# Optimization experiments

Hardware: AMD Instinct MI355X
Metric: run time of the kernel (lower is better)

The kernel has to match this reference:

```python
import jax, jax.numpy as jnp
import numpy as np

B, T, S = 128, 500, 200   # batch, seq_len, num_skills
E, H = 100, 100           # embed_dim, lstm hidden


def setup_inputs() -> dict:
    key = jax.random.key(0)
    ks = jax.random.split(key, 8)
    skill = jax.random.randint(ks[0], (B, T), 0, S)
    bit = jax.random.randint(ks[1], (B, T), 0, 2)
    # one-hot interaction: position 2*skill + (0 if correct else 1)
    x = jax.nn.one_hot(skill * 2 + bit, 2 * S, dtype=jnp.float32)
    qi = jax.random.randint(ks[2], (B, T), 0, S)
    q = jax.nn.one_hot(qi, S, dtype=jnp.float32)
    delta = jnp.zeros((B, T, 1), jnp.float32)  # unused in no_tempo model
    Wx = jax.random.normal(ks[3], (2 * S, E), jnp.float32) * 0.05
    bx = jnp.zeros((E,), jnp.float32)
    # LSTM input dim = E + 3 (correct/incorrect/total count feats)
    lstm_k = jax.random.normal(ks[4], (E + 3, 4 * H), jnp.float32) * 0.05
    lstm_rk = jax.random.normal(ks[5], (H, 4 * H), jnp.float32) * 0.05
    # keras unit_forget_bias: forget-gate bias section = 1 (gate order i,f,c,o)
    lstm_b = jnp.concatenate([jnp.zeros(H), jnp.ones(H), jnp.zeros(2 * H)]).astype(jnp.float32)
    Wo = jax.random.normal(ks[6], (H, S), jnp.float32) * 0.05
    bo = jnp.zeros((S,), jnp.float32)
    return {"x": x, "delta": delta, "q": q, "Wx": Wx, "bx": bx,
            "lstm_k": lstm_k, "lstm_rk": lstm_rk, "lstm_b": lstm_b,
            "Wo": Wo, "bo": bo}


def _forward(x, q, Wx, bx, lstm_k, lstm_rk, lstm_b, Wo, bo):
    mask = jnp.any(x != 0, axis=-1)              # [B,T] keras Masking(0)
    embed_x = x @ Wx + bx                        # [B,T,E]
    xt = jnp.swapaxes(x, 0, 1)                   # [T,B,2S]
    mt = jnp.swapaxes(mask, 0, 1)                # [T,B]

    # CountStateRNNCell: state = sum(x_t)*prev + x_t ; masked steps pass state through
    def count_step(c, inp):
        x_t, m_t = inp
        new = jnp.sum(x_t, axis=-1, keepdims=True) * c + x_t
        c = jnp.where(m_t[:, None], new, c)
        return c, c

    c0 = jnp.zeros((x.shape[0], x.shape[-1]), x.dtype)
    _, counts = jax.lax.scan(count_step, c0, (xt, mt))
    count_t = jnp.log1p(jnp.swapaxes(counts, 0, 1))  # [B,T,2S]

    idx = jnp.argmax(x, axis=-1) // 2                # skill index [B,T]
    # one_hot * count + reduce_sum  ==  gather
    cc = jnp.take_along_axis(count_t, (idx * 2)[..., None], axis=-1)      # correct
    ic = jnp.take_along_axis(count_t, (idx * 2 + 1)[..., None], axis=-1)  # incorrect
    # count_format='binary' hits the typo'd else-branch -> all_count (3 feats)
    count_feat = jnp.concatenate([cc, ic, cc + ic], axis=-1)              # [B,T,3]

    x_c_t = jnp.concatenate([embed_x, count_feat], axis=-1)               # [B,T,E+3]
    zt = jnp.swapaxes(x_c_t @ lstm_k + lstm_b, 0, 1)                      # [T,B,4H]

    def lstm_step(carry, inp):
        h, c = carry
        z_t, m_t = inp
        z = z_t + h @ lstm_rk
        i, f, g, o = jnp.split(z, 4, axis=-1)
        c_new = jax.nn.sigmoid(f) * c + jax.nn.sigmoid(i) * jnp.tanh(g)
        h_new = jax.nn.sigmoid(o) * jnp.tanh(c_new)
        m = m_t[:, None]
        h = jnp.where(m, h_new, h)
        c = jnp.where(m, c_new, c)
        return (h, c), h

    h0 = jnp.zeros((x.shape[0], H), x.dtype)
    _, hs = jax.lax.scan(lstm_step, (h0, h0), (zt, mt))
    h_seq = jnp.swapaxes(hs, 0, 1)                                        # [B,T,H]

    # dropout = identity (inference); Dense(1, kernel=1, bias=0) = sum over skills
    y = jax.nn.sigmoid(h_seq @ Wo + bo) * q
    return jnp.sum(y, axis=-1, keepdims=True)                             # [B,T,1]


def reference(x, delta, q, Wx, bx, lstm_k, lstm_rk, lstm_b, Wo, bo):
    return _forward(x, q, Wx, bx, lstm_k, lstm_rk, lstm_b, Wo, bo)
```

## Files before the change

### kernel.cpp

```cpp
#include <hip/hip_runtime.h>
#include <hip/hip_bf16.h>
#include <hip/hip_fp16.h>

#define TB 128
#define TT 500
#define TS 200
#define TE 100
#define TH 100
#define NCLS 400
#define NG   400
#define BT   (TB*TT)
#define BLK  448

typedef _Float16 h8 __attribute__((ext_vector_type(8)));
union HU { float4 f4; __half hs[8]; };

__device__ __forceinline__ float frcp(float x) { return __builtin_amdgcn_rcpf(x); }
__device__ __forceinline__ float fsig(float x) { return frcp(1.f + __expf(-x)); }
__device__ __forceinline__ float ftanh(float x) { float e = __expf(2.f * x); return 1.f - 2.f * frcp(e + 1.f); }

__device__ __forceinline__ void barrier_lds() {
  asm volatile("s_waitcnt lgkmcnt(0)\n\ts_barrier" ::: "memory");
}

#define QXOR1(d, s) d = __int_as_float(__builtin_amdgcn_mov_dpp(__float_as_int(s), 177, 0xf, 0xf, true))
#define QXOR2(d, s) d = __int_as_float(__builtin_amdgcn_mov_dpp(__float_as_int(s),  78, 0xf, 0xf, true))
#define QXOR3(d, s) d = __int_as_float(__builtin_amdgcn_mov_dpp(__float_as_int(s),  27, 0xf, 0xf, true))

__global__ void k_compress(const float* __restrict__ x, const float* __restrict__ q,
                           int* __restrict__ idx2, int* __restrict__ qi) {
  int gid  = blockIdx.x * blockDim.x + threadIdx.x;
  int wave = gid >> 6;
  int lane = threadIdx.x & 63;
  if (wave >= BT) return;

  const float4* xr = (const float4*)(x + (size_t)wave * NCLS);
  int li = -1;
  {
    float4 v = xr[lane];
    if (v.x > 0.5f) li = lane * 4 + 0;
    if (v.y > 0.5f) li = lane * 4 + 1;
    if (v.z > 0.5f) li = lane * 4 + 2;
    if (v.w > 0.5f) li = lane * 4 + 3;
    int ci = 64 + lane;
    if (ci < 100) {
      float4 w = xr[ci];
      if (w.x > 0.5f) li = ci * 4 + 0;
      if (w.y > 0.5f) li = ci * 4 + 1;
      if (w.z > 0.5f) li = ci * 4 + 2;
      if (w.w > 0.5f) li = ci * 4 + 3;
    }
  }
  #pragma unroll
  for (int off = 32; off; off >>= 1) li = max(li, __shfl_xor(li, off));

  const float4* qr = (const float4*)(q + (size_t)wave * TS);
  int qj = -1;
  if (lane < 50) {
    float4 v = qr[lane];
    if (v.x > 0.5f) qj = lane * 4 + 0;
    if (v.y > 0.5f) qj = lane * 4 + 1;
    if (v.z > 0.5f) qj = lane * 4 + 2;
    if (v.w > 0.5f) qj = lane * 4 + 3;
  }
  #pragma unroll
  for (int off = 32; off; off >>= 1) qj = max(qj, __shfl_xor(qj, off));

  if (lane == 0) { idx2[wave] = li; qi[wave] = qj; }
}

__global__ void k_counts(const int* __restrict__ idx2, float2* __restrict__ ccg) {
  __shared__ int ids[TT];
  int b = blockIdx.x, tid = threadIdx.x;
  for (int i = tid; i < TT; i += 512) ids[i] = idx2[(size_t)b * TT + i];
  __syncthreads();
  if (tid < TT) {
    int s2 = ids[tid] & ~1;
    int c0 = 0, c1 = 0;
    for (int tp = 0; tp <= tid; ++tp) {
      int v = ids[tp];
      c0 += (v == s2);
      c1 += (v == s2 + 1);
    }
    ccg[(size_t)b * TT + tid] =
        make_float2(__logf(1.f + (float)c0), __logf(1.f + (float)c1));
  }
}

__global__ void k_precompute(const float* __restrict__ Wx, const float* __restrict__ bx,
                             const float* __restrict__ K, const float* __restrict__ lb,
                             const float* __restrict__ Wo, const float* __restrict__ R,
                             float* __restrict__ Gq, float* __restrict__ baseq,
                             float* __restrict__ c0q, float* __restrict__ c1q,
                             float* __restrict__ WoT, float4* __restrict__ Bfrag) {
  int bid = blockIdx.x, tid = threadIdx.x;
  if (bid < NCLS) {
    if (tid < NG) {
      float acc = 0.0f;
      for (int e = 0; e < TE; ++e) acc = fmaf(Wx[bid * TE + e], K[e * NG + tid], acc);
      int g = tid / 100, u = tid % 100;
      int cp = (u >> 2) * 16 + (u & 3) * 4 + g;
      Gq[bid * NG + cp] = acc;
    }
  } else if (bid == NCLS) {
    if (tid < NG) {
      float acc = lb[tid];
      for (int e = 0; e < TE; ++e) acc = fmaf(bx[e], K[e * NG + tid], acc);
      int g = tid / 100, u = tid % 100;
      int cp = (u >> 2) * 16 + (u & 3) * 4 + g;
      baseq[cp] = acc;
      c0q[cp]   = K[100 * NG + tid] + K[102 * NG + tid];
      c1q[cp]   = K[101 * NG + tid] + K[102 * NG + tid];
    }
  } else {
    int id = (bid - NCLS - 1) * 512 + tid;
    if (id < TS * TH) {
      int s = id / TH, k = id % TH;
      WoT[id] = Wo[k * TS + s];
    } else {
      int id2 = id - TS * TH;
      if (id2 < 6400) {
        int lane = id2 & 63, ks = (id2 >> 6) & 3, tile = id2 >> 8;
        int qq = lane & 15, cgrp = lane >> 4;
        int col = (qq & 3) * 100 + tile * 4 + (qq >> 2);
        HU uu;
        #pragma unroll
        for (int j = 0; j < 8; ++j) {
          int k = ks * 32 + cgrp * 8 + j;
          float v = (k < TH) ? R[k * NG + col] : 0.0f;
          uu.hs[j] = __float2half_rn(v);
        }
        Bfrag[id2] = uu.f4;
      }
    }
  }
}

#define AW(N, V) asm volatile("v_accvgpr_write_b32 a" #N ", %0" :: "v"(V) : "a" #N)
#define AW4(N0,N1,N2,N3, F) do { AW(N0,(F).x); AW(N1,(F).y); AW(N2,(F).z); AW(N3,(F).w); } while(0)

#define CLOBS \
  "a0","a1","a2","a3","a4","a5","a6","a7","a8","a9","a10","a11","a12","a13", \
  "a14","a15","a16","a17","a18","a19","a20","a21","a22","a23","a24","a25",   \
  "a26","a27","a28","a29","a30","a31","a32","a33","a34","a35","a36","a37",   \
  "a38","a39","a40","a41","a42","a43","a44","a45","a46","a47","a48","a49",   \
  "a50","a51","a52","a53","a54","a55","a56","a57","a58","a59","a60","a61",   \
  "a62","a63","a64","a65","a66","a67","a68","a69","a70","a71","a72","a73",   \
  "a74","a75","a76","a77","a78","a79","a80","a81","a82","a83"

#define MFMA16(Z0,Z1,Z2,Z3, FA0,FA1,FA2,FA3)                          \
  asm volatile(                                                       \
    "s_nop 1\n\t"                                                     \
    "v_mfma_f32_16x16x32_f16 a[64:67], %4, a[0:3],   a[80:83]\n\t"    \
    "v_mfma_f32_16x16x32_f16 a[68:71], %4, a[16:19], a[80:83]\n\t"    \
    "v_mfma_f32_16x16x32_f16 a[72:75], %4, a[32:35], a[80:83]\n\t"    \
    "v_mfma_f32_16x16x32_f16 a[76:79], %4, a[48:51], a[80:83]\n\t"    \
    "v_mfma_f32_16x16x32_f16 a[64:67], %5, a[4:7],   a[64:67]\n\t"    \
    "v_mfma_f32_16x16x32_f16 a[68:71], %5, a[20:23], a[68:71]\n\t"    \
    "v_mfma_f32_16x16x32_f16 a[72:75], %5, a[36:39], a[72:75]\n\t"    \
    "v_mfma_f32_16x16x32_f16 a[76:79], %5, a[52:55], a[76:79]\n\t"    \
    "v_mfma_f32_16x16x32_f16 a[64:67], %6, a[8:11],  a[64:67]\n\t"    \
    "v_mfma_f32_16x16x32_f16 a[68:71], %6, a[24:27], a[68:71]\n\t"    \
    "v_mfma_f32_16x16x32_f16 a[72:75], %6, a[40:43], a[72:75]\n\t"    \
    "v_mfma_f32_16x16x32_f16 a[76:79], %6, a[56:59], a[76:79]\n\t"    \
    "v_mfma_f32_16x16x32_f16 a[64:67], %7, a[12:15], a[64:67]\n\t"    \
    "v_mfma_f32_16x16x32_f16 a[68:71], %7, a[28:31], a[68:71]\n\t"    \
    "v_mfma_f32_16x16x32_f16 a[72:75], %7, a[44:47], a[72:75]\n\t"    \
    "v_mfma_f32_16x16x32_f16 a[76:79], %7, a[60:63], a[76:79]\n\t"    \
    "s_nop 7\n\ts_nop 7\n\ts_nop 7\n\t"                               \
    "v_accvgpr_read_b32 %0, a64\n\t"                                  \
    "v_accvgpr_read_b32 %1, a68\n\t"                                  \
    "v_accvgpr_read_b32 %2, a72\n\t"                                  \
    "v_accvgpr_read_b32 %3, a76"                                      \
    : "=v"(Z0), "=v"(Z1), "=v"(Z2), "=v"(Z3)                          \
    : "v"(FA0), "v"(FA1), "v"(FA2), "v"(FA3)                          \
    : CLOBS)

__global__ void __attribute__((amdgpu_flat_work_group_size(BLK, BLK)))
k_lstm(const int* __restrict__ idx2, const float* __restrict__ Gq,
       const float* __restrict__ baseq, const float* __restrict__ c0q,
       const float* __restrict__ c1q, const float4* __restrict__ Bfrag,
       const float2* __restrict__ ccg, float* __restrict__ h_seq) {
  __shared__ __align__(16) __half hbuf[2][128];
  __shared__ int idx_ls[TT];

  int b = blockIdx.x, tid = threadIdx.x;
  int w = tid >> 6, lane = tid & 63;
  int g3 = lane & 3, cg = lane >> 4, qd = (lane >> 2) & 3;

  for (int i = tid; i < TT; i += BLK) idx_ls[i] = idx2[(size_t)b * TT + i];
  if (tid < 128) { hbuf[0][tid] = __float2half(0.f); hbuf[1][tid] = __float2half(0.f); }

  int tS0 = (w < 6) ? 4 * w     : 24;
  int tS1 = (w < 6) ? 4 * w + 1 : 24;
  int tS2 = (w < 6) ? 4 * w + 2 : 24;
  int tS3 = (w < 6) ? 4 * w + 3 : 24;

  int gcol = (w < 6) ? (64 * w + lane)
                     : (24 * 16 + (lane & 15));
  float basej = baseq[gcol], c0j = c0q[gcol], c1j = c1q[gcol];
  int u_wr = 16 * w + 4 * cg + qd;
  bool wr = (g3 == 0) && (((w < 6) ? u_wr : (96 + qd)) < TH) && !(w == 6 && cg != 0);
  int u_fin = (w < 6) ? u_wr : (96 + qd);

  {
    float4 f;
    f = Bfrag[(tS0 * 4 + 0) * 64 + lane]; AW4(0,1,2,3, f);
    f = Bfrag[(tS0 * 4 + 1) * 64 + lane]; AW4(4,5,6,7, f);
    f = Bfrag[(tS0 * 4 + 2) * 64 + lane]; AW4(8,9,10,11, f);
    f = Bfrag[(tS0 * 4 + 3) * 64 + lane]; AW4(12,13,14,15, f);
    f = Bfrag[(tS1 * 4 + 0) * 64 + lane]; AW4(16,17,18,19, f);
    f = Bfrag[(tS1 * 4 + 1) * 64 + lane]; AW4(20,21,22,23, f);
    f = Bfrag[(tS1 * 4 + 2) * 64 + lane]; AW4(24,25,26,27, f);
    f = Bfrag[(tS1 * 4 + 3) * 64 + lane]; AW4(28,29,30,31, f);
    f = Bfrag[(tS2 * 4 + 0) * 64 + lane]; AW4(32,33,34,35, f);
    f = Bfrag[(tS2 * 4 + 1) * 64 + lane]; AW4(36,37,38,39, f);
    f = Bfrag[(tS2 * 4 + 2) * 64 + lane]; AW4(40,41,42,43, f);
    f = Bfrag[(tS2 * 4 + 3) * 64 + lane]; AW4(44,45,46,47, f);
    f = Bfrag[(tS3 * 4 + 0) * 64 + lane]; AW4(48,49,50,51, f);
    f = Bfrag[(tS3 * 4 + 1) * 64 + lane]; AW4(52,53,54,55, f);
    f = Bfrag[(tS3 * 4 + 2) * 64 + lane]; AW4(56,57,58,59, f);
    f = Bfrag[(tS3 * 4 + 3) * 64 + lane]; AW4(60,61,62,63, f);
    float zf = 0.0f;
    AW(80, zf); AW(81, zf); AW(82, zf); AW(83, zf);
  }
  asm volatile("" ::: CLOBS);

  float c_reg = 0.f;
  __syncthreads();

  const float2* ccg_b = ccg + (size_t)b * TT;
  float gA = Gq[(size_t)idx_ls[0] * NG + gcol];
  float gB = Gq[(size_t)idx_ls[1] * NG + gcol];
  float2 ccA = ccg_b[0], ccB = ccg_b[1];

  float* hout = h_seq + (size_t)b * TT * TH;

  #define STEP(T_, PAR, GV, CCV)                                               \
  { const int t_ = (T_);                                                       \
    barrier_lds();                   \
    const h8* hrow = (const h8*)(&hbuf[(PAR) ^ 1][0]);                         \
    h8 fa0 = hrow[cg], fa1 = hrow[4 + cg], fa2 = hrow[8 + cg], fa3 = hrow[12 + cg]; \
    float z0, z1, z2, z3;                                                      \
    MFMA16(z0, z1, z2, z3, fa0, fa1, fa2, fa3);                                \
    float zlo = (cg & 1) ? z1 : z0;                                            \
    float zhi = (cg & 1) ? z3 : z2;                                            \
    float zsel = (cg & 2) ? zhi : zlo;                                         \
    float2 cc = (CCV);                                                         \
    int tnx = (t_ + 2 < TT) ? t_ + 2 : TT - 1;                                 \
    float z = zsel + (GV) + basej + cc.x * c0j + cc.y * c1j;                   \
    (GV) = Gq[(size_t)idx_ls[tnx] * NG + gcol];          \
    (CCV) = ccg_b[tnx];                                                        \
    float arg = (g3 == 2) ? (z + z) : (-z);                                    \
    float E = __expf(arg);                                                     \
    float r = frcp(1.f + E);                                                   \
    float act = (g3 == 2) ? fmaf(-2.f, r, 1.f) : r;                            \
    float x1, x2, x3;                                                          \
    QXOR1(x1, act); QXOR2(x2, act); QXOR3(x3, act);                            \
    c_reg = fmaf(x1, c_reg, act * x2);               \
    float hn = x3 * ftanh(c_reg);                                              \
    if (wr) {                                                                  \
      hbuf[PAR][u_fin] = __float2half_rn(hn);       \
      hout[(size_t)t_ * TH + u_fin] = hn;                \
    }                                                                          \
  }

  for (int t2 = 0; t2 < TT; t2 += 2) {
    STEP(t2, 0, gA, ccA);
    STEP(t2 + 1, 1, gB, ccB);
  }
  #undef STEP
}

__global__ void k_out(const float* __restrict__ h_seq, const float* __restrict__ WoT,
                      const float* __restrict__ bo, const int* __restrict__ qi,
                      float* __restrict__ out) {
  int gid  = blockIdx.x * blockDim.x + threadIdx.x;
  int wave = gid >> 6;
  int lane = threadIdx.x & 63;
  if (wave >= BT) return;
  int s = qi[wave];
  const float4* h4 = (const float4*)(h_seq + (size_t)wave * TH);
  const float4* w4 = (const float4*)(WoT + (size_t)s * TH);
  float acc = 0.0f;
  if (lane < TH / 4) {
    float4 h = h4[lane];
    float4 w = w4[lane];
    acc = h.x * w.x + h.y * w.y + h.z * w.z + h.w * w.w;
  }
  #pragma unroll
  for (int off = 32; off; off >>= 1) acc += __shfl_xor(acc, off);
  if (lane == 0) out[wave] = fsig(acc + bo[s]);
}

extern "C" void kernel_launch(void* const* d_in, const int* in_sizes, int n_in,
                              void* d_out, int out_size, void* d_ws, size_t ws_size,
                              hipStream_t stream) {
  const float* x    = (const float*)d_in[0];
  const float* q    = (const float*)d_in[2];
  const float* Wx   = (const float*)d_in[3];
  const float* bx   = (const float*)d_in[4];
  const float* K    = (const float*)d_in[5];
  const float* R    = (const float*)d_in[6];
  const float* lb   = (const float*)d_in[7];
  const float* Wo   = (const float*)d_in[8];
  const float* bo   = (const float*)d_in[9];
  float* out = (float*)d_out;

  float* ws = (float*)d_ws;
  float*  Gq     = ws;
  float*  baseq  = ws + 160000;
  float*  c0q    = ws + 160400;
  float*  c1q    = ws + 160800;
  float*  WoT    = ws + 161200;
  float4* Bfrag  = (float4*)(ws + 181200);
  int*    idx2   = (int*)(ws + 206800);
  int*    qi     = (int*)(ws + 270800);
  float2* ccg    = (float2*)(ws + 334800);
  float*  h_seq  = ws + 462800;

  k_compress<<<BT / 4, 256, 0, stream>>>(x, q, idx2, qi);

  k_counts<<<TB, 512, 0, stream>>>(idx2, ccg);

  int tail_blocks = (TS * TH + 6400 + 511) / 512;
  k_precompute<<<NCLS + 1 + tail_blocks, 512, 0, stream>>>(Wx, bx, K, lb, Wo, R,
                                                           Gq, baseq, c0q, c1q, WoT, Bfrag);

  k_lstm<<<TB, BLK, 0, stream>>>(idx2, Gq, baseq, c0q, c1q, Bfrag, ccg, h_seq);

  k_out<<<BT / 4, 256, 0, stream>>>(h_seq, WoT, bo, qi, out);
}
```

Measured before the change: 304.1 us.

## Process two batch sequences per LSTM block using spare MFMA rows

The recurrent LSTM kernel now handles two batch elements per workgroup and launches half as many blocks. The A operand rows of the 16x16 MFMA carry both sequences' hidden states, and each lane runs the gate activations for two outputs. The point is to use MFMA rows that previously computed nothing and to halve the number of serial-recurrence blocks. In exchange each lane does twice the elementwise and gather work per step, and only 64 blocks are active on the GPU.

New measurement: 361.2 us. 18.8% more time.

```diff
diff --git a/kernel.cpp b/kernel.cpp
--- a/kernel.cpp
+++ b/kernel.cpp
@@ -181,27 +181,33 @@
        const float* __restrict__ baseq, const float* __restrict__ c0q,
        const float* __restrict__ c1q, const float4* __restrict__ Bfrag,
        const float2* __restrict__ ccg, float* __restrict__ h_seq) {
-  __shared__ __align__(16) __half hbuf[2][128];
-  __shared__ int idx_ls[TT];
-
-  int b = blockIdx.x, tid = threadIdx.x;
+  __shared__ __align__(16) __half hbuf[2][2][128];
+  __shared__ int idx_ls[2][TT];
+
+  int bid = blockIdx.x, tid = threadIdx.x;
   int w = tid >> 6, lane = tid & 63;
-  int g3 = lane & 3, cg = lane >> 4, qd = (lane >> 2) & 3;
-
-  for (int i = tid; i < TT; i += BLK) idx_ls[i] = idx2[(size_t)b * TT + i];
-  if (tid < 128) { hbuf[0][tid] = __float2half(0.f); hbuf[1][tid] = __float2half(0.f); }
-
-  int tS0 = (w < 6) ? 4 * w     : 24;
-  int tS1 = (w < 6) ? 4 * w + 1 : 24;
-  int tS2 = (w < 6) ? 4 * w + 2 : 24;
-  int tS3 = (w < 6) ? 4 * w + 3 : 24;
-
-  int gcol = (w < 6) ? (64 * w + lane)
-                     : (24 * 16 + (lane & 15));
-  float basej = baseq[gcol], c0j = c0q[gcol], c1j = c1q[gcol];
-  int u_wr = 16 * w + 4 * cg + qd;
-  bool wr = (g3 == 0) && (((w < 6) ? u_wr : (96 + qd)) < TH) && !(w == 6 && cg != 0);
-  int u_fin = (w < 6) ? u_wr : (96 + qd);
+  int q = lane & 15, g3 = lane & 3, cg = lane >> 4, qd = (lane >> 2) & 3;
+  int eA   = (lane >> 3) & 1;
+  int eact = cg >> 1;
+  int s1 = cg & 1, s2 = s1 + 2;
+
+  for (int i = tid; i < TT; i += BLK) {
+    idx_ls[0][i] = idx2[(size_t)(2 * bid) * TT + i];
+    idx_ls[1][i] = idx2[(size_t)(2 * bid + 1) * TT + i];
+  }
+  { __half* hb = &hbuf[0][0][0];
+    for (int i = tid; i < 512; i += BLK) hb[i] = __float2half(0.f); }
+
+  int tS0 = min(4 * w + 0, 24), tS1 = min(4 * w + 1, 24);
+  int tS2 = min(4 * w + 2, 24), tS3 = min(4 * w + 3, 24);
+  int tU1 = 4 * w + s1, tU2 = 4 * w + s2;
+  int tC1 = min(tU1, 24), tC2 = min(tU2, 24);
+  int gcol1 = tC1 * 16 + q, gcol2 = tC2 * 16 + q;
+  float base1 = baseq[gcol1], c01 = c0q[gcol1], c11 = c1q[gcol1];
+  float base2 = baseq[gcol2], c02 = c0q[gcol2], c12 = c1q[gcol2];
+  int u1 = tU1 * 4 + qd, u2 = tU2 * 4 + qd;
+  bool wr1 = (g3 == 0) && (u1 < TH);
+  bool wr2 = (g3 == 0) && (u2 < TH);
 
   {
     float4 f;
@@ -226,50 +232,65 @@
   }
   asm volatile("" ::: CLOBS);
 
-  float c_reg = 0.f;
+  float c_reg1 = 0.f, c_reg2 = 0.f;
   __syncthreads();
 
-  const float2* ccg_b = ccg + (size_t)b * TT;
-  float gA = Gq[(size_t)idx_ls[0] * NG + gcol];
-  float gB = Gq[(size_t)idx_ls[1] * NG + gcol];
-  float2 ccA = ccg_b[0], ccB = ccg_b[1];
-
-  float* hout = h_seq + (size_t)b * TT * TH;
-
-  #define STEP(T_, PAR, GV, CCV)                                               \
-  { const int t_ = (T_);                                                       \
-    barrier_lds();                   \
-    const h8* hrow = (const h8*)(&hbuf[(PAR) ^ 1][0]);                         \
-    h8 fa0 = hrow[cg], fa1 = hrow[4 + cg], fa2 = hrow[8 + cg], fa3 = hrow[12 + cg]; \
-    float z0, z1, z2, z3;                                                      \
-    MFMA16(z0, z1, z2, z3, fa0, fa1, fa2, fa3);                                \
-    float zlo = (cg & 1) ? z1 : z0;                                            \
-    float zhi = (cg & 1) ? z3 : z2;                                            \
-    float zsel = (cg & 2) ? zhi : zlo;                                         \
-    float2 cc = (CCV);                                                         \
-    int tnx = (t_ + 2 < TT) ? t_ + 2 : TT - 1;                                 \
-    float z = zsel + (GV) + basej + cc.x * c0j + cc.y * c1j;                   \
-    (GV) = Gq[(size_t)idx_ls[tnx] * NG + gcol];          \
-    (CCV) = ccg_b[tnx];                                                        \
-    float arg = (g3 == 2) ? (z + z) : (-z);                                    \
+  const int* idxe = idx_ls[eact];
+  const float2* ccg_e = ccg + (size_t)(2 * bid + eact) * TT;
+  float* hout_e = h_seq + (size_t)(2 * bid + eact) * TT * TH;
+
+  float g1A = Gq[(size_t)idxe[0] * NG + gcol1];
+  float g2A = Gq[(size_t)idxe[0] * NG + gcol2];
+  float g1B = Gq[(size_t)idxe[1] * NG + gcol1];
+  float g2B = Gq[(size_t)idxe[1] * NG + gcol2];
+  float2 ccA = ccg_e[0], ccB = ccg_e[1];
+
+  #define ACT(ZZ, CREG, HN)                                                    \
+  { float arg = (g3 == 2) ? ((ZZ) + (ZZ)) : (-(ZZ));                           \
     float E = __expf(arg);                                                     \
     float r = frcp(1.f + E);                                                   \
     float act = (g3 == 2) ? fmaf(-2.f, r, 1.f) : r;                            \
     float x1, x2, x3;                                                          \
     QXOR1(x1, act); QXOR2(x2, act); QXOR3(x3, act);                            \
-    c_reg = fmaf(x1, c_reg, act * x2);               \
-    float hn = x3 * ftanh(c_reg);                                              \
-    if (wr) {                                                                  \
-      hbuf[PAR][u_fin] = __float2half_rn(hn);       \
-      hout[(size_t)t_ * TH + u_fin] = hn;                \
+    (CREG) = fmaf(x1, (CREG), act * x2);   \
+    (HN) = x3 * ftanh(CREG); }
+
+  #define STEP(T_, PAR, G1, G2, CCV)                                           \
+  { const int t_ = (T_);                                                       \
+    barrier_lds();                   \
+    const h8* hrowA = (const h8*)(&hbuf[eA][(PAR) ^ 1][0]);                    \
+    h8 fa0 = hrowA[cg], fa1 = hrowA[4 + cg], fa2 = hrowA[8 + cg], fa3 = hrowA[12 + cg]; \
+    float z0, z1, z2, z3;                                                      \
+    MFMA16(z0, z1, z2, z3, fa0, fa1, fa2, fa3);                                \
+    float zs1 = s1 ? z1 : z0;                                   \
+    float zs2 = s1 ? z3 : z2;                               \
+    float2 cc = (CCV);                                                         \
+    int tnx = (t_ + 2 < TT) ? t_ + 2 : TT - 1;                                 \
+    float zz1 = zs1 + (G1) + base1 + cc.x * c01 + cc.y * c11;                  \
+    float zz2 = zs2 + (G2) + base2 + cc.x * c02 + cc.y * c12;                  \
+    int idn = idxe[tnx];                                                       \
+    (G1) = Gq[(size_t)idn * NG + gcol1];                   \
+    (G2) = Gq[(size_t)idn * NG + gcol2];                                       \
+    (CCV) = ccg_e[tnx];                                                        \
+    float hn1, hn2;                                                            \
+    ACT(zz1, c_reg1, hn1);                                                     \
+    ACT(zz2, c_reg2, hn2);                                                     \
+    if (wr1) {                                                                 \
+      hbuf[eact][PAR][u1] = __float2half_rn(hn1);                              \
+      hout_e[(size_t)t_ * TH + u1] = hn1;                \
     }                                                                          \
+    if (wr2) {                                                                 \
+      hbuf[eact][PAR][u2] = __float2half_rn(hn2);                              \
+      hout_e[(size_t)t_ * TH + u2] = hn2;                                      \
+    }                                                                          \
   }
 
   for (int t2 = 0; t2 < TT; t2 += 2) {
-    STEP(t2, 0, gA, ccA);
-    STEP(t2 + 1, 1, gB, ccB);
+    STEP(t2, 0, g1A, g2A, ccA);
+    STEP(t2 + 1, 1, g1B, g2B, ccB);
   }
   #undef STEP
+  #undef ACT
 }
 
 __global__ void k_out(const float* __restrict__ h_seq, const float* __restrict__ WoT,
@@ -327,7 +348,7 @@
   k_precompute<<<NCLS + 1 + tail_blocks, 512, 0, stream>>>(Wx, bx, K, lb, Wo, R,
                                                            Gq, baseq, c0q, c1q, WoT, Bfrag);
 
-  k_lstm<<<TB, BLK, 0, stream>>>(idx2, Gq, baseq, c0q, c1q, Bfrag, ccg, h_seq);
+  k_lstm<<<TB / 2, BLK, 0, stream>>>(idx2, Gq, baseq, c0q, c1q, Bfrag, ccg, h_seq);
 
   k_out<<<BT / 4, 256, 0, stream>>>(h_seq, WoT, bo, qi, out);
 }
```

## Redistribute LSTM gate tiles across four waves with seven MFMA tiles each

Applied to the files above, without the earlier changes.

The recurrent LSTM kernel drops from 7 waves (448 threads) to 4 waves (256 threads). Each wave now holds seven 16-column gate tiles in accumulation registers instead of four, issues 28 MFMAs per step, and processes two gate columns per lane. Fewer waves make the per-step barrier cheaper and reduce LDS reads of h. In exchange each wave's serial chain per timestep gets longer (more MFMAs and two activation passes), and AGPR use rises to 144 registers.

New measurement: 375.1 us. 1.23x slower.

```diff
diff --git a/kernel.cpp b/kernel.cpp
--- a/kernel.cpp
+++ b/kernel.cpp
@@ -10,7 +10,7 @@
 #define NCLS 400
 #define NG   400
 #define BT   (TB*TT)
-#define BLK  448
+#define BLK  256
 
 typedef _Float16 h8 __attribute__((ext_vector_type(8)));
 union HU { float4 f4; __half hs[8]; };
@@ -146,33 +146,54 @@
   "a38","a39","a40","a41","a42","a43","a44","a45","a46","a47","a48","a49",   \
   "a50","a51","a52","a53","a54","a55","a56","a57","a58","a59","a60","a61",   \
   "a62","a63","a64","a65","a66","a67","a68","a69","a70","a71","a72","a73",   \
-  "a74","a75","a76","a77","a78","a79","a80","a81","a82","a83"
-
-#define MFMA16(Z0,Z1,Z2,Z3, FA0,FA1,FA2,FA3)                          \
+  "a74","a75","a76","a77","a78","a79","a80","a81","a82","a83","a84","a85",   \
+  "a86","a87","a88","a89","a90","a91","a92","a93","a94","a95","a96","a97",   \
+  "a98","a99","a100","a101","a102","a103","a104","a105","a106","a107",       \
+  "a108","a109","a110","a111","a112","a113","a114","a115","a116","a117",     \
+  "a118","a119","a120","a121","a122","a123","a124","a125","a126","a127",     \
+  "a128","a129","a130","a131","a132","a133","a134","a135","a136","a137",     \
+  "a138","a139","a140","a141","a142","a143"
+
+#define MFMA28(Z0,Z1,Z2,Z3,Z4,Z5,Z6, FA0,FA1,FA2,FA3)                \
   asm volatile(                                                       \
     "s_nop 1\n\t"                                                     \
-    "v_mfma_f32_16x16x32_f16 a[64:67], %4, a[0:3],   a[80:83]\n\t"    \
-    "v_mfma_f32_16x16x32_f16 a[68:71], %4, a[16:19], a[80:83]\n\t"    \
-    "v_mfma_f32_16x16x32_f16 a[72:75], %4, a[32:35], a[80:83]\n\t"    \
-    "v_mfma_f32_16x16x32_f16 a[76:79], %4, a[48:51], a[80:83]\n\t"    \
-    "v_mfma_f32_16x16x32_f16 a[64:67], %5, a[4:7],   a[64:67]\n\t"    \
-    "v_mfma_f32_16x16x32_f16 a[68:71], %5, a[20:23], a[68:71]\n\t"    \
-    "v_mfma_f32_16x16x32_f16 a[72:75], %5, a[36:39], a[72:75]\n\t"    \
-    "v_mfma_f32_16x16x32_f16 a[76:79], %5, a[52:55], a[76:79]\n\t"    \
-    "v_mfma_f32_16x16x32_f16 a[64:67], %6, a[8:11],  a[64:67]\n\t"    \
-    "v_mfma_f32_16x16x32_f16 a[68:71], %6, a[24:27], a[68:71]\n\t"    \
-    "v_mfma_f32_16x16x32_f16 a[72:75], %6, a[40:43], a[72:75]\n\t"    \
-    "v_mfma_f32_16x16x32_f16 a[76:79], %6, a[56:59], a[76:79]\n\t"    \
-    "v_mfma_f32_16x16x32_f16 a[64:67], %7, a[12:15], a[64:67]\n\t"    \
-    "v_mfma_f32_16x16x32_f16 a[68:71], %7, a[28:31], a[68:71]\n\t"    \
-    "v_mfma_f32_16x16x32_f16 a[72:75], %7, a[44:47], a[72:75]\n\t"    \
-    "v_mfma_f32_16x16x32_f16 a[76:79], %7, a[60:63], a[76:79]\n\t"    \
-    "s_nop 7\n\ts_nop 7\n\ts_nop 7\n\t"                               \
-    "v_accvgpr_read_b32 %0, a64\n\t"                                  \
-    "v_accvgpr_read_b32 %1, a68\n\t"                                  \
-    "v_accvgpr_read_b32 %2, a72\n\t"                                  \
-    "v_accvgpr_read_b32 %3, a76"                                      \
-    : "=v"(Z0), "=v"(Z1), "=v"(Z2), "=v"(Z3)                          \
+    "v_mfma_f32_16x16x32_f16 a[112:115], %7, a[0:3],    a[140:143]\n\t" \
+    "v_mfma_f32_16x16x32_f16 a[116:119], %7, a[16:19],  a[140:143]\n\t" \
+    "v_mfma_f32_16x16x32_f16 a[120:123], %7, a[32:35],  a[140:143]\n\t" \
+    "v_mfma_f32_16x16x32_f16 a[124:127], %7, a[48:51],  a[140:143]\n\t" \
+    "v_mfma_f32_16x16x32_f16 a[128:131], %7, a[64:67],  a[140:143]\n\t" \
+    "v_mfma_f32_16x16x32_f16 a[132:135], %7, a[80:83],  a[140:143]\n\t" \
+    "v_mfma_f32_16x16x32_f16 a[136:139], %7, a[96:99],  a[140:143]\n\t" \
+    "v_mfma_f32_16x16x32_f16 a[112:115], %8, a[4:7],    a[112:115]\n\t" \
+    "v_mfma_f32_16x16x32_f16 a[116:119], %8, a[20:23],  a[116:119]\n\t" \
+    "v_mfma_f32_16x16x32_f16 a[120:123], %8, a[36:39],  a[120:123]\n\t" \
+    "v_mfma_f32_16x16x32_f16 a[124:127], %8, a[52:55],  a[124:127]\n\t" \
+    "v_mfma_f32_16x16x32_f16 a[128:131], %8, a[68:71],  a[128:131]\n\t" \
+    "v_mfma_f32_16x16x32_f16 a[132:135], %8, a[84:87],  a[132:135]\n\t" \
+    "v_mfma_f32_16x16x32_f16 a[136:139], %8, a[100:103],a[136:139]\n\t" \
+    "v_mfma_f32_16x16x32_f16 a[112:115], %9, a[8:11],   a[112:115]\n\t" \
+    "v_mfma_f32_16x16x32_f16 a[116:119], %9, a[24:27],  a[116:119]\n\t" \
+    "v_mfma_f32_16x16x32_f16 a[120:123], %9, a[40:43],  a[120:123]\n\t" \
+    "v_mfma_f32_16x16x32_f16 a[124:127], %9, a[56:59],  a[124:127]\n\t" \
+    "v_mfma_f32_16x16x32_f16 a[128:131], %9, a[72:75],  a[128:131]\n\t" \
+    "v_mfma_f32_16x16x32_f16 a[132:135], %9, a[88:91],  a[132:135]\n\t" \
+    "v_mfma_f32_16x16x32_f16 a[136:139], %9, a[104:107],a[136:139]\n\t" \
+    "v_mfma_f32_16x16x32_f16 a[112:115], %10, a[12:15], a[112:115]\n\t" \
+    "v_mfma_f32_16x16x32_f16 a[116:119], %10, a[28:31], a[116:119]\n\t" \
+    "v_mfma_f32_16x16x32_f16 a[120:123], %10, a[44:47], a[120:123]\n\t" \
+    "v_mfma_f32_16x16x32_f16 a[124:127], %10, a[60:63], a[124:127]\n\t" \
+    "v_mfma_f32_16x16x32_f16 a[128:131], %10, a[76:79], a[128:131]\n\t" \
+    "v_mfma_f32_16x16x32_f16 a[132:135], %10, a[92:95], a[132:135]\n\t" \
+    "v_mfma_f32_16x16x32_f16 a[136:139], %10, a[108:111],a[136:139]\n\t" \
+    "v_accvgpr_read_b32 %0, a112\n\t"                                 \
+    "v_accvgpr_read_b32 %1, a116\n\t"                                 \
+    "v_accvgpr_read_b32 %2, a120\n\t"                                 \
+    "v_accvgpr_read_b32 %3, a124\n\t"                                 \
+    "v_accvgpr_read_b32 %4, a128\n\t"                                 \
+    "s_nop 7\n\ts_nop 7\n\t"                                          \
+    "v_accvgpr_read_b32 %5, a132\n\t"                                 \
+    "v_accvgpr_read_b32 %6, a136"                                     \
+    : "=v"(Z0), "=v"(Z1), "=v"(Z2), "=v"(Z3), "=v"(Z4), "=v"(Z5), "=v"(Z6) \
     : "v"(FA0), "v"(FA1), "v"(FA2), "v"(FA3)                          \
     : CLOBS)
 
@@ -186,90 +207,120 @@
 
   int b = blockIdx.x, tid = threadIdx.x;
   int w = tid >> 6, lane = tid & 63;
-  int g3 = lane & 3, cg = lane >> 4, qd = (lane >> 2) & 3;
+  int q = lane & 15, g3 = lane & 3, cg = lane >> 4, qd = (lane >> 2) & 3;
 
   for (int i = tid; i < TT; i += BLK) idx_ls[i] = idx2[(size_t)b * TT + i];
-  if (tid < 128) { hbuf[0][tid] = __float2half(0.f); hbuf[1][tid] = __float2half(0.f); }
-
-  int tS0 = (w < 6) ? 4 * w     : 24;
-  int tS1 = (w < 6) ? 4 * w + 1 : 24;
-  int tS2 = (w < 6) ? 4 * w + 2 : 24;
-  int tS3 = (w < 6) ? 4 * w + 3 : 24;
-
-  int gcol = (w < 6) ? (64 * w + lane)
-                     : (24 * 16 + (lane & 15));
-  float basej = baseq[gcol], c0j = c0q[gcol], c1j = c1q[gcol];
-  int u_wr = 16 * w + 4 * cg + qd;
-  bool wr = (g3 == 0) && (((w < 6) ? u_wr : (96 + qd)) < TH) && !(w == 6 && cg != 0);
-  int u_fin = (w < 6) ? u_wr : (96 + qd);
+  { __half* hb = &hbuf[0][0];
+    for (int i = tid; i < 256; i += BLK) hb[i] = __float2half(0.f); }
+
+  int t0 = min(6 * w + 0, 24), t1 = min(6 * w + 1, 24), t2 = min(6 * w + 2, 24);
+  int t3 = min(6 * w + 3, 24), t4 = min(6 * w + 4, 24), t5 = min(6 * w + 5, 24);
+  int t6 = min(6 * w + 6, 24);
+
+  int tileA = 6 * w + cg;
+  int tileBu = 6 * w + 4 + cg;
+  int tileB = min(tileBu, 24);
+  int gcolA = tileA * 16 + q, gcolB = tileB * 16 + q;
+  float baseA = baseq[gcolA], c0A = c0q[gcolA], c1A = c1q[gcolA];
+  float baseB = baseq[gcolB], c0B = c0q[gcolB], c1B = c1q[gcolB];
+  int uA = tileA * 4 + qd, uB = tileB * 4 + qd;
+  bool ownB = (w == 3) ? (cg < 3) : (cg < 2);
+  bool wrA = (g3 == 0);
+  bool wrB = (g3 == 0) && ownB;
 
   {
     float4 f;
-    f = Bfrag[(tS0 * 4 + 0) * 64 + lane]; AW4(0,1,2,3, f);
-    f = Bfrag[(tS0 * 4 + 1) * 64 + lane]; AW4(4,5,6,7, f);
-    f = Bfrag[(tS0 * 4 + 2) * 64 + lane]; AW4(8,9,10,11, f);
-    f = Bfrag[(tS0 * 4 + 3) * 64 + lane]; AW4(12,13,14,15, f);
-    f = Bfrag[(tS1 * 4 + 0) * 64 + lane]; AW4(16,17,18,19, f);
-    f = Bfrag[(tS1 * 4 + 1) * 64 + lane]; AW4(20,21,22,23, f);
-    f = Bfrag[(tS1 * 4 + 2) * 64 + lane]; AW4(24,25,26,27, f);
-    f = Bfrag[(tS1 * 4 + 3) * 64 + lane]; AW4(28,29,30,31, f);
-    f = Bfrag[(tS2 * 4 + 0) * 64 + lane]; AW4(32,33,34,35, f);
-    f = Bfrag[(tS2 * 4 + 1) * 64 + lane]; AW4(36,37,38,39, f);
-    f = Bfrag[(tS2 * 4 + 2) * 64 + lane]; AW4(40,41,42,43, f);
-    f = Bfrag[(tS2 * 4 + 3) * 64 + lane]; AW4(44,45,46,47, f);
-    f = Bfrag[(tS3 * 4 + 0) * 64 + lane]; AW4(48,49,50,51, f);
-    f = Bfrag[(tS3 * 4 + 1) * 64 + lane]; AW4(52,53,54,55, f);
-    f = Bfrag[(tS3 * 4 + 2) * 64 + lane]; AW4(56,57,58,59, f);
-    f = Bfrag[(tS3 * 4 + 3) * 64 + lane]; AW4(60,61,62,63, f);
+    f = Bfrag[(t0 * 4 + 0) * 64 + lane]; AW4(0,1,2,3, f);
+    f = Bfrag[(t0 * 4 + 1) * 64 + lane]; AW4(4,5,6,7, f);
+    f = Bfrag[(t0 * 4 + 2) * 64 + lane]; AW4(8,9,10,11, f);
+    f = Bfrag[(t0 * 4 + 3) * 64 + lane]; AW4(12,13,14,15, f);
+    f = Bfrag[(t1 * 4 + 0) * 64 + lane]; AW4(16,17,18,19, f);
+    f = Bfrag[(t1 * 4 + 1) * 64 + lane]; AW4(20,21,22,23, f);
+    f = Bfrag[(t1 * 4 + 2) * 64 + lane]; AW4(24,25,26,27, f);
+    f = Bfrag[(t1 * 4 + 3) * 64 + lane]; AW4(28,29,30,31, f);
+    f = Bfrag[(t2 * 4 + 0) * 64 + lane]; AW4(32,33,34,35, f);
+    f = Bfrag[(t2 * 4 + 1) * 64 + lane]; AW4(36,37,38,39, f);
+    f = Bfrag[(t2 * 4 + 2) * 64 + lane]; AW4(40,41,42,43, f);
+    f = Bfrag[(t2 * 4 + 3) * 64 + lane]; AW4(44,45,46,47, f);
+    f = Bfrag[(t3 * 4 + 0) * 64 + lane]; AW4(48,49,50,51, f);
+    f = Bfrag[(t3 * 4 + 1) * 64 + lane]; AW4(52,53,54,55, f);
+    f = Bfrag[(t3 * 4 + 2) * 64 + lane]; AW4(56,57,58,59, f);
+    f = Bfrag[(t3 * 4 + 3) * 64 + lane]; AW4(60,61,62,63, f);
+    f = Bfrag[(t4 * 4 + 0) * 64 + lane]; AW4(64,65,66,67, f);
+    f = Bfrag[(t4 * 4 + 1) * 64 + lane]; AW4(68,69,70,71, f);
+    f = Bfrag[(t4 * 4 + 2) * 64 + lane]; AW4(72,73,74,75, f);
+    f = Bfrag[(t4 * 4 + 3) * 64 + lane]; AW4(76,77,78,79, f);
+    f = Bfrag[(t5 * 4 + 0) * 64 + lane]; AW4(80,81,82,83, f);
+    f = Bfrag[(t5 * 4 + 1) * 64 + lane]; AW4(84,85,86,87, f);
+    f = Bfrag[(t5 * 4 + 2) * 64 + lane]; AW4(88,89,90,91, f);
+    f = Bfrag[(t5 * 4 + 3) * 64 + lane]; AW4(92,93,94,95, f);
+    f = Bfrag[(t6 * 4 + 0) * 64 + lane]; AW4(96,97,98,99, f);
+    f = Bfrag[(t6 * 4 + 1) * 64 + lane]; AW4(100,101,102,103, f);
+    f = Bfrag[(t6 * 4 + 2) * 64 + lane]; AW4(104,105,106,107, f);
+    f = Bfrag[(t6 * 4 + 3) * 64 + lane]; AW4(108,109,110,111, f);
     float zf = 0.0f;
-    AW(80, zf); AW(81, zf); AW(82, zf); AW(83, zf);
+    AW(140, zf); AW(141, zf); AW(142, zf); AW(143, zf);
   }
   asm volatile("" ::: CLOBS);
 
-  float c_reg = 0.f;
+  float c_regA = 0.f, c_regB = 0.f;
   __syncthreads();
 
   const float2* ccg_b = ccg + (size_t)b * TT;
-  float gA = Gq[(size_t)idx_ls[0] * NG + gcol];
-  float gB = Gq[(size_t)idx_ls[1] * NG + gcol];
+  float* hout = h_seq + (size_t)b * TT * TH;
+
+  float gA1 = Gq[(size_t)idx_ls[0] * NG + gcolA];
+  float gA2 = Gq[(size_t)idx_ls[0] * NG + gcolB];
+  float gB1 = Gq[(size_t)idx_ls[1] * NG + gcolA];
+  float gB2 = Gq[(size_t)idx_ls[1] * NG + gcolB];
   float2 ccA = ccg_b[0], ccB = ccg_b[1];
 
-  float* hout = h_seq + (size_t)b * TT * TH;
-
-  #define STEP(T_, PAR, GV, CCV)                                               \
-  { const int t_ = (T_);                                                       \
-    barrier_lds();                   \
-    const h8* hrow = (const h8*)(&hbuf[(PAR) ^ 1][0]);                         \
-    h8 fa0 = hrow[cg], fa1 = hrow[4 + cg], fa2 = hrow[8 + cg], fa3 = hrow[12 + cg]; \
-    float z0, z1, z2, z3;                                                      \
-    MFMA16(z0, z1, z2, z3, fa0, fa1, fa2, fa3);                                \
-    float zlo = (cg & 1) ? z1 : z0;                                            \
-    float zhi = (cg & 1) ? z3 : z2;                                            \
-    float zsel = (cg & 2) ? zhi : zlo;                                         \
-    float2 cc = (CCV);                                                         \
-    int tnx = (t_ + 2 < TT) ? t_ + 2 : TT - 1;                                 \
-    float z = zsel + (GV) + basej + cc.x * c0j + cc.y * c1j;                   \
-    (GV) = Gq[(size_t)idx_ls[tnx] * NG + gcol];          \
-    (CCV) = ccg_b[tnx];                                                        \
-    float arg = (g3 == 2) ? (z + z) : (-z);                                    \
+  #define ACT(ZZ, CREG, HN)                                                    \
+  { float arg = (g3 == 2) ? ((ZZ) + (ZZ)) : (-(ZZ));                           \
     float E = __expf(arg);                                                     \
     float r = frcp(1.f + E);                                                   \
     float act = (g3 == 2) ? fmaf(-2.f, r, 1.f) : r;                            \
     float x1, x2, x3;                                                          \
     QXOR1(x1, act); QXOR2(x2, act); QXOR3(x3, act);                            \
-    c_reg = fmaf(x1, c_reg, act * x2);               \
-    float hn = x3 * ftanh(c_reg);                                              \
-    if (wr) {                                                                  \
-      hbuf[PAR][u_fin] = __float2half_rn(hn);       \
-      hout[(size_t)t_ * TH + u_fin] = hn;                \
+    (CREG) = fmaf(x1, (CREG), act * x2);   \
+    (HN) = x3 * ftanh(CREG); }
+
+  #define STEP(T_, PAR, G1, G2, CCV)                                           \
+  { const int t_ = (T_);                                                       \
+    barrier_lds();                   \
+    const h8* hrow = (const h8*)(&hbuf[(PAR) ^ 1][0]);                         \
+    h8 fa0 = hrow[cg], fa1 = hrow[4 + cg], fa2 = hrow[8 + cg], fa3 = hrow[12 + cg]; \
+    float z0, z1, z2, z3, z4, z5, z6;                                          \
+    MFMA28(z0, z1, z2, z3, z4, z5, z6, fa0, fa1, fa2, fa3);                    \
+    float zA = (cg == 0) ? z0 : (cg == 1) ? z1 : (cg == 2) ? z2 : z3;          \
+    float zB = (cg == 0) ? z4 : (cg == 1) ? z5 : z6;                           \
+    float2 cc = (CCV);                                                         \
+    int tnx = (t_ + 2 < TT) ? t_ + 2 : TT - 1;                                 \
+    float zzA = zA + (G1) + baseA + cc.x * c0A + cc.y * c1A;                   \
+    float zzB = zB + (G2) + baseB + cc.x * c0B + cc.y * c1B;                   \
+    int idn = idx_ls[tnx];                                                     \
+    (G1) = Gq[(size_t)idn * NG + gcolA];                   \
+    (G2) = Gq[(size_t)idn * NG + gcolB];                                       \
+    (CCV) = ccg_b[tnx];                                                        \
+    float hnA, hnB;                                                            \
+    ACT(zzA, c_regA, hnA);                                                     \
+    ACT(zzB, c_regB, hnB);                                                     \
+    if (wrA) {                                                                 \
+      hbuf[PAR][uA] = __float2half_rn(hnA);                                    \
+      hout[(size_t)t_ * TH + uA] = hnA;                  \
     }                                                                          \
-  }
-
-  for (int t2 = 0; t2 < TT; t2 += 2) {
-    STEP(t2, 0, gA, ccA);
-    STEP(t2 + 1, 1, gB, ccB);
+    if (wrB) {                                                                 \
+      hbuf[PAR][uB] = __float2half_rn(hnB);                                    \
+      hout[(size_t)t_ * TH + uB] = hnB;                                        \
+    }                                                                          \
+  }
+
+  for (int t2p = 0; t2p < TT; t2p += 2) {
+    STEP(t2p, 0, gA1, gA2, ccA);
+    STEP(t2p + 1, 1, gB1, gB2, ccB);
   }
   #undef STEP
+  #undef ACT
 }
 
 __global__ void k_out(const float* __restrict__ h_seq, const float* __restrict__ WoT,
```

## Redistribute LSTM gate tiles across eight waves with three MFMA tiles each

Applied to the files above, without the earlier changes.

The recurrent LSTM kernel grows from 7 to 8 waves per block. Waves 0-6 each compute 3 column tiles of the recurrent matmul instead of 4, and wave 7 takes the last 4 tiles. This shortens the serial MFMA chain on the per-step critical path for most waves, at the cost of more threads per block, an uneven last wave, and one branch per step.

After: 285.0 us. 1.07x faster.

```diff
diff --git a/kernel.cpp b/kernel.cpp
--- a/kernel.cpp
+++ b/kernel.cpp
@@ -10,7 +10,7 @@
 #define NCLS 400
 #define NG   400
 #define BT   (TB*TT)
-#define BLK  448
+#define BLK  512
 
 typedef _Float16 h8 __attribute__((ext_vector_type(8)));
 union HU { float4 f4; __half hs[8]; };
@@ -148,33 +148,56 @@
   "a62","a63","a64","a65","a66","a67","a68","a69","a70","a71","a72","a73",   \
   "a74","a75","a76","a77","a78","a79","a80","a81","a82","a83"
 
-#define MFMA16(Z0,Z1,Z2,Z3, FA0,FA1,FA2,FA3)                          \
-  asm volatile(                                                       \
-    "s_nop 1\n\t"                                                     \
-    "v_mfma_f32_16x16x32_f16 a[64:67], %4, a[0:3],   a[80:83]\n\t"    \
-    "v_mfma_f32_16x16x32_f16 a[68:71], %4, a[16:19], a[80:83]\n\t"    \
-    "v_mfma_f32_16x16x32_f16 a[72:75], %4, a[32:35], a[80:83]\n\t"    \
-    "v_mfma_f32_16x16x32_f16 a[76:79], %4, a[48:51], a[80:83]\n\t"    \
-    "v_mfma_f32_16x16x32_f16 a[64:67], %5, a[4:7],   a[64:67]\n\t"    \
-    "v_mfma_f32_16x16x32_f16 a[68:71], %5, a[20:23], a[68:71]\n\t"    \
-    "v_mfma_f32_16x16x32_f16 a[72:75], %5, a[36:39], a[72:75]\n\t"    \
-    "v_mfma_f32_16x16x32_f16 a[76:79], %5, a[52:55], a[76:79]\n\t"    \
-    "v_mfma_f32_16x16x32_f16 a[64:67], %6, a[8:11],  a[64:67]\n\t"    \
-    "v_mfma_f32_16x16x32_f16 a[68:71], %6, a[24:27], a[68:71]\n\t"    \
-    "v_mfma_f32_16x16x32_f16 a[72:75], %6, a[40:43], a[72:75]\n\t"    \
-    "v_mfma_f32_16x16x32_f16 a[76:79], %6, a[56:59], a[76:79]\n\t"    \
-    "v_mfma_f32_16x16x32_f16 a[64:67], %7, a[12:15], a[64:67]\n\t"    \
-    "v_mfma_f32_16x16x32_f16 a[68:71], %7, a[28:31], a[68:71]\n\t"    \
-    "v_mfma_f32_16x16x32_f16 a[72:75], %7, a[44:47], a[72:75]\n\t"    \
-    "v_mfma_f32_16x16x32_f16 a[76:79], %7, a[60:63], a[76:79]\n\t"    \
-    "s_nop 7\n\ts_nop 7\n\ts_nop 7\n\t"                               \
-    "v_accvgpr_read_b32 %0, a64\n\t"                                  \
-    "v_accvgpr_read_b32 %1, a68\n\t"                                  \
-    "v_accvgpr_read_b32 %2, a72\n\t"                                  \
-    "v_accvgpr_read_b32 %3, a76"                                      \
-    : "=v"(Z0), "=v"(Z1), "=v"(Z2), "=v"(Z3)                          \
-    : "v"(FA0), "v"(FA1), "v"(FA2), "v"(FA3)                          \
-    : CLOBS)
+#define MK0_4(FA) asm volatile("s_nop 1\n\t" \
+  "v_mfma_f32_16x16x32_f16 a[64:67], %0, a[0:3],   a[80:83]\n\t" \
+  "v_mfma_f32_16x16x32_f16 a[68:71], %0, a[16:19], a[80:83]\n\t" \
+  "v_mfma_f32_16x16x32_f16 a[72:75], %0, a[32:35], a[80:83]\n\t" \
+  "v_mfma_f32_16x16x32_f16 a[76:79], %0, a[48:51], a[80:83]" :: "v"(FA) : CLOBS)
+#define MK1_4(FA) asm volatile("s_nop 1\n\t" \
+  "v_mfma_f32_16x16x32_f16 a[64:67], %0, a[4:7],   a[64:67]\n\t" \
+  "v_mfma_f32_16x16x32_f16 a[68:71], %0, a[20:23], a[68:71]\n\t" \
+  "v_mfma_f32_16x16x32_f16 a[72:75], %0, a[36:39], a[72:75]\n\t" \
+  "v_mfma_f32_16x16x32_f16 a[76:79], %0, a[52:55], a[76:79]" :: "v"(FA) : CLOBS)
+#define MK2_4(FA) asm volatile("s_nop 1\n\t" \
+  "v_mfma_f32_16x16x32_f16 a[64:67], %0, a[8:11],  a[64:67]\n\t" \
+  "v_mfma_f32_16x16x32_f16 a[68:71], %0, a[24:27], a[68:71]\n\t" \
+  "v_mfma_f32_16x16x32_f16 a[72:75], %0, a[40:43], a[72:75]\n\t" \
+  "v_mfma_f32_16x16x32_f16 a[76:79], %0, a[56:59], a[76:79]" :: "v"(FA) : CLOBS)
+#define MK3_4(FA) asm volatile("s_nop 1\n\t" \
+  "v_mfma_f32_16x16x32_f16 a[64:67], %0, a[12:15], a[64:67]\n\t" \
+  "v_mfma_f32_16x16x32_f16 a[68:71], %0, a[28:31], a[68:71]\n\t" \
+  "v_mfma_f32_16x16x32_f16 a[72:75], %0, a[44:47], a[72:75]\n\t" \
+  "v_mfma_f32_16x16x32_f16 a[76:79], %0, a[60:63], a[76:79]" :: "v"(FA) : CLOBS)
+#define MK0_3(FA) asm volatile("s_nop 1\n\t" \
+  "v_mfma_f32_16x16x32_f16 a[64:67], %0, a[0:3],   a[80:83]\n\t" \
+  "v_mfma_f32_16x16x32_f16 a[68:71], %0, a[16:19], a[80:83]\n\t" \
+  "v_mfma_f32_16x16x32_f16 a[72:75], %0, a[32:35], a[80:83]" :: "v"(FA) : CLOBS)
+#define MK1_3(FA) asm volatile("s_nop 1\n\t" \
+  "v_mfma_f32_16x16x32_f16 a[64:67], %0, a[4:7],   a[64:67]\n\t" \
+  "v_mfma_f32_16x16x32_f16 a[68:71], %0, a[20:23], a[68:71]\n\t" \
+  "v_mfma_f32_16x16x32_f16 a[72:75], %0, a[36:39], a[72:75]" :: "v"(FA) : CLOBS)
+#define MK2_3(FA) asm volatile("s_nop 1\n\t" \
+  "v_mfma_f32_16x16x32_f16 a[64:67], %0, a[8:11],  a[64:67]\n\t" \
+  "v_mfma_f32_16x16x32_f16 a[68:71], %0, a[24:27], a[68:71]\n\t" \
+  "v_mfma_f32_16x16x32_f16 a[72:75], %0, a[40:43], a[72:75]" :: "v"(FA) : CLOBS)
+#define MK3_3(FA) asm volatile("s_nop 1\n\t" \
+  "v_mfma_f32_16x16x32_f16 a[64:67], %0, a[12:15], a[64:67]\n\t" \
+  "v_mfma_f32_16x16x32_f16 a[68:71], %0, a[28:31], a[68:71]\n\t" \
+  "v_mfma_f32_16x16x32_f16 a[72:75], %0, a[44:47], a[72:75]" :: "v"(FA) : CLOBS)
+
+#define RD4(Z0,Z1,Z2,Z3) asm volatile( \
+  "s_nop 7\n\ts_nop 7\n\ts_nop 7\n\t" \
+  "v_accvgpr_read_b32 %0, a64\n\t" \
+  "v_accvgpr_read_b32 %1, a68\n\t" \
+  "v_accvgpr_read_b32 %2, a72\n\t" \
+  "v_accvgpr_read_b32 %3, a76" \
+  : "=v"(Z0), "=v"(Z1), "=v"(Z2), "=v"(Z3) :: CLOBS)
+#define RD3(Z0,Z1,Z2) asm volatile( \
+  "s_nop 7\n\ts_nop 7\n\ts_nop 7\n\t" \
+  "v_accvgpr_read_b32 %0, a64\n\t" \
+  "v_accvgpr_read_b32 %1, a68\n\t" \
+  "v_accvgpr_read_b32 %2, a72" \
+  : "=v"(Z0), "=v"(Z1), "=v"(Z2) :: CLOBS)
 
 __global__ void __attribute__((amdgpu_flat_work_group_size(BLK, BLK)))
 k_lstm(const int* __restrict__ idx2, const float* __restrict__ Gq,
@@ -186,41 +209,40 @@
 
   int b = blockIdx.x, tid = threadIdx.x;
   int w = tid >> 6, lane = tid & 63;
-  int g3 = lane & 3, cg = lane >> 4, qd = (lane >> 2) & 3;
+  int q = lane & 15, g3 = lane & 3, cg = lane >> 4, qd = (lane >> 2) & 3;
 
   for (int i = tid; i < TT; i += BLK) idx_ls[i] = idx2[(size_t)b * TT + i];
-  if (tid < 128) { hbuf[0][tid] = __float2half(0.f); hbuf[1][tid] = __float2half(0.f); }
-
-  int tS0 = (w < 6) ? 4 * w     : 24;
-  int tS1 = (w < 6) ? 4 * w + 1 : 24;
-  int tS2 = (w < 6) ? 4 * w + 2 : 24;
-  int tS3 = (w < 6) ? 4 * w + 3 : 24;
-
-  int gcol = (w < 6) ? (64 * w + lane)
-                     : (24 * 16 + (lane & 15));
-  float basej = baseq[gcol], c0j = c0q[gcol], c1j = c1q[gcol];
-  int u_wr = 16 * w + 4 * cg + qd;
-  bool wr = (g3 == 0) && (((w < 6) ? u_wr : (96 + qd)) < TH) && !(w == 6 && cg != 0);
-  int u_fin = (w < 6) ? u_wr : (96 + qd);
+  { __half* hb = &hbuf[0][0];
+    if (tid < 256) hb[tid] = __float2half(0.f); }
+
+  int t0 = (w < 7) ? 3 * w : 21;
+  int t1 = t0 + 1, t2 = t0 + 2;
+  int t3 = 24;
+  bool own = (w == 7) || (cg < 3);
+  int tileA = t0 + ((w == 7) ? cg : min(cg, 2));
+  int gcolA = tileA * 16 + q;
+  float basej = baseq[gcolA], c0j = c0q[gcolA], c1j = c1q[gcolA];
+  int uA = tileA * 4 + qd;
+  bool wr = (g3 == 0) && own;
 
   {
     float4 f;
-    f = Bfrag[(tS0 * 4 + 0) * 64 + lane]; AW4(0,1,2,3, f);
-    f = Bfrag[(tS0 * 4 + 1) * 64 + lane]; AW4(4,5,6,7, f);
-    f = Bfrag[(tS0 * 4 + 2) * 64 + lane]; AW4(8,9,10,11, f);
-    f = Bfrag[(tS0 * 4 + 3) * 64 + lane]; AW4(12,13,14,15, f);
-    f = Bfrag[(tS1 * 4 + 0) * 64 + lane]; AW4(16,17,18,19, f);
-    f = Bfrag[(tS1 * 4 + 1) * 64 + lane]; AW4(20,21,22,23, f);
-    f = Bfrag[(tS1 * 4 + 2) * 64 + lane]; AW4(24,25,26,27, f);
-    f = Bfrag[(tS1 * 4 + 3) * 64 + lane]; AW4(28,29,30,31, f);
-    f = Bfrag[(tS2 * 4 + 0) * 64 + lane]; AW4(32,33,34,35, f);
-    f = Bfrag[(tS2 * 4 + 1) * 64 + lane]; AW4(36,37,38,39, f);
-    f = Bfrag[(tS2 * 4 + 2) * 64 + lane]; AW4(40,41,42,43, f);
-    f = Bfrag[(tS2 * 4 + 3) * 64 + lane]; AW4(44,45,46,47, f);
-    f = Bfrag[(tS3 * 4 + 0) * 64 + lane]; AW4(48,49,50,51, f);
-    f = Bfrag[(tS3 * 4 + 1) * 64 + lane]; AW4(52,53,54,55, f);
-    f = Bfrag[(tS3 * 4 + 2) * 64 + lane]; AW4(56,57,58,59, f);
-    f = Bfrag[(tS3 * 4 + 3) * 64 + lane]; AW4(60,61,62,63, f);
+    f = Bfrag[(t0 * 4 + 0) * 64 + lane]; AW4(0,1,2,3, f);
+    f = Bfrag[(t0 * 4 + 1) * 64 + lane]; AW4(4,5,6,7, f);
+    f = Bfrag[(t0 * 4 + 2) * 64 + lane]; AW4(8,9,10,11, f);
+    f = Bfrag[(t0 * 4 + 3) * 64 + lane]; AW4(12,13,14,15, f);
+    f = Bfrag[(t1 * 4 + 0) * 64 + lane]; AW4(16,17,18,19, f);
+    f = Bfrag[(t1 * 4 + 1) * 64 + lane]; AW4(20,21,22,23, f);
+    f = Bfrag[(t1 * 4 + 2) * 64 + lane]; AW4(24,25,26,27, f);
+    f = Bfrag[(t1 * 4 + 3) * 64 + lane]; AW4(28,29,30,31, f);
+    f = Bfrag[(t2 * 4 + 0) * 64 + lane]; AW4(32,33,34,35, f);
+    f = Bfrag[(t2 * 4 + 1) * 64 + lane]; AW4(36,37,38,39, f);
+    f = Bfrag[(t2 * 4 + 2) * 64 + lane]; AW4(40,41,42,43, f);
+    f = Bfrag[(t2 * 4 + 3) * 64 + lane]; AW4(44,45,46,47, f);
+    f = Bfrag[(t3 * 4 + 0) * 64 + lane]; AW4(48,49,50,51, f);
+    f = Bfrag[(t3 * 4 + 1) * 64 + lane]; AW4(52,53,54,55, f);
+    f = Bfrag[(t3 * 4 + 2) * 64 + lane]; AW4(56,57,58,59, f);
+    f = Bfrag[(t3 * 4 + 3) * 64 + lane]; AW4(60,61,62,63, f);
     float zf = 0.0f;
     AW(80, zf); AW(81, zf); AW(82, zf); AW(83, zf);
   }
@@ -230,11 +252,21 @@
   __syncthreads();
 
   const float2* ccg_b = ccg + (size_t)b * TT;
-  float gA = Gq[(size_t)idx_ls[0] * NG + gcol];
-  float gB = Gq[(size_t)idx_ls[1] * NG + gcol];
+  float* hout = h_seq + (size_t)b * TT * TH;
+
+  float gA = Gq[(size_t)idx_ls[0] * NG + gcolA];
+  float gB = Gq[(size_t)idx_ls[1] * NG + gcolA];
   float2 ccA = ccg_b[0], ccB = ccg_b[1];
 
-  float* hout = h_seq + (size_t)b * TT * TH;
+  #define ACT(ZZ, CREG, HN)                                                    \
+  { float arg = (g3 == 2) ? ((ZZ) + (ZZ)) : (-(ZZ));                           \
+    float E = __expf(arg);                                                     \
+    float r = frcp(1.f + E);                                                   \
+    float act = (g3 == 2) ? fmaf(-2.f, r, 1.f) : r;                            \
+    float x1, x2, x3;                                                          \
+    QXOR1(x1, act); QXOR2(x2, act); QXOR3(x3, act);                            \
+    (CREG) = fmaf(x1, (CREG), act * x2);   \
+    (HN) = x3 * ftanh(CREG); }
 
   #define STEP(T_, PAR, GV, CCV)                                               \
   { const int t_ = (T_);                                                       \
@@ -242,34 +274,34 @@
     const h8* hrow = (const h8*)(&hbuf[(PAR) ^ 1][0]);                         \
     h8 fa0 = hrow[cg], fa1 = hrow[4 + cg], fa2 = hrow[8 + cg], fa3 = hrow[12 + cg]; \
     float z0, z1, z2, z3;                                                      \
-    MFMA16(z0, z1, z2, z3, fa0, fa1, fa2, fa3);                                \
-    float zlo = (cg & 1) ? z1 : z0;                                            \
-    float zhi = (cg & 1) ? z3 : z2;                                            \
-    float zsel = (cg & 2) ? zhi : zlo;                                         \
+    if (w == 7) {                                                              \
+      MK0_4(fa0); MK1_4(fa1); MK2_4(fa2); MK3_4(fa3);                          \
+      RD4(z0, z1, z2, z3);                                                     \
+    } else {                                                                   \
+      MK0_3(fa0); MK1_3(fa1); MK2_3(fa2); MK3_3(fa3);                          \
+      RD3(z0, z1, z2); z3 = z2;                                                \
+    }                                                                          \
+    float zA = (cg == 0) ? z0 : (cg == 1) ? z1 : (cg == 2) ? z2 : z3;          \
     float2 cc = (CCV);                                                         \
     int tnx = (t_ + 2 < TT) ? t_ + 2 : TT - 1;                                 \
-    float z = zsel + (GV) + basej + cc.x * c0j + cc.y * c1j;                   \
-    (GV) = Gq[(size_t)idx_ls[tnx] * NG + gcol];          \
+    float zz = zA + (GV) + basej + cc.x * c0j + cc.y * c1j;                    \
+    int idn = idx_ls[tnx];                                                     \
+    (GV) = Gq[(size_t)idn * NG + gcolA];                   \
     (CCV) = ccg_b[tnx];                                                        \
-    float arg = (g3 == 2) ? (z + z) : (-z);                                    \
-    float E = __expf(arg);                                                     \
-    float r = frcp(1.f + E);                                                   \
-    float act = (g3 == 2) ? fmaf(-2.f, r, 1.f) : r;                            \
-    float x1, x2, x3;                                                          \
-    QXOR1(x1, act); QXOR2(x2, act); QXOR3(x3, act);                            \
-    c_reg = fmaf(x1, c_reg, act * x2);               \
-    float hn = x3 * ftanh(c_reg);                                              \
+    float hn;                                                                  \
+    ACT(zz, c_reg, hn);                                                        \
     if (wr) {                                                                  \
-      hbuf[PAR][u_fin] = __float2half_rn(hn);       \
-      hout[(size_t)t_ * TH + u_fin] = hn;                \
+      hbuf[PAR][uA] = __float2half_rn(hn);                                     \
+      hout[(size_t)t_ * TH + uA] = hn;                   \
     }                                                                          \
   }
 
-  for (int t2 = 0; t2 < TT; t2 += 2) {
-    STEP(t2, 0, gA, ccA);
-    STEP(t2 + 1, 1, gB, ccB);
+  for (int t2p = 0; t2p < TT; t2p += 2) {
+    STEP(t2p, 0, gA, ccA);
+    STEP(t2p + 1, 1, gB, ccB);
   }
   #undef STEP
+  #undef ACT
 }
 
 __global__ void k_out(const float* __restrict__ h_seq, const float* __restrict__ WoT,
```
